# Kernel tuning notes

Measured on AMD Instinct MI355X. Metric: run time of the kernel, lower is better.

Reference implementation:

```python
import jax, jax.numpy as jnp
import numpy as np

HIDDEN = 768

def setup_inputs() -> dict:
    key = jax.random.key(0)
    k1, k2, k3 = jax.random.split(key, 3)
    x = jax.random.normal(k1, (8, 2048, HIDDEN), dtype=jnp.float32)
    # nn.Linear(hidden, 3*hidden): weight [3H, H], bias [3H]; torch init ~ U(-1/sqrt(H), 1/sqrt(H))
    bound = 1.0 / np.sqrt(HIDDEN)
    W = jax.random.uniform(k2, (3 * HIDDEN, HIDDEN), dtype=jnp.float32, minval=-bound, maxval=bound)
    b = jax.random.uniform(k3, (3 * HIDDEN,), dtype=jnp.float32, minval=-bound, maxval=bound)
    return {"x": x, "W": W, "b": b}

def reference(x, W, b):
    # qkv: [B, N, 3H]
    qkv = jnp.einsum('bnd,hd->bnh', x, W) + b
    q, k, v = jnp.split(qkv, 3, axis=-1)  # each [B, N, H]
    # NOTE: original module applies NO 1/sqrt(d) scaling — kept faithful.
    weights = jnp.einsum('bnd,bmd->bnm', q, k)          # [B, N, N]
    weights = jax.nn.softmax(weights, axis=-1)
    out = jnp.einsum('bnm,bmd->bnd', weights, v)        # [B, N, H]
    return out
```

## Files before the change

### kernel.cpp

```cpp
#include <hip/hip_runtime.h>


typedef short    s16x8 __attribute__((ext_vector_type(8)));
typedef _Float16 h16x8 __attribute__((ext_vector_type(8)));
typedef _Float16 h16x4 __attribute__((ext_vector_type(4)));
typedef float    f32x4 __attribute__((ext_vector_type(4)));

__device__ __forceinline__ unsigned short f2bf(float x) {
    unsigned u = __float_as_uint(x);
    u += 0x7fffu + ((u >> 16) & 1u);
    return (unsigned short)(u >> 16);
}
__device__ __forceinline__ float bf2f(unsigned short h) {
    return __uint_as_float(((unsigned)h) << 16);
}
__device__ __forceinline__ unsigned short f2h(float x) {
    _Float16 h = (_Float16)x;
    unsigned short u;
    __builtin_memcpy(&u, &h, 2);
    return u;
}
__device__ __forceinline__ h16x8 as_h(s16x8 v) {
    h16x8 r; __builtin_memcpy(&r, &v, 16); return r;
}

__device__ __forceinline__ void gld16(const void* g, void* l) {
    __builtin_amdgcn_global_load_lds(
        (const __attribute__((address_space(1))) unsigned int*)(unsigned long long)g,
        (__attribute__((address_space(3))) unsigned int*)(unsigned)(unsigned long long)l,
        16, 0, 0);
}

template<bool FP16>
__device__ __forceinline__ f32x4 mma(s16x8 a, s16x8 b, f32x4 c) {
    if constexpr (FP16)
        return __builtin_amdgcn_mfma_f32_16x16x32_f16(as_h(a), as_h(b), c, 0, 0, 0);
    else
        return __builtin_amdgcn_mfma_f32_16x16x32_bf16(a, b, c, 0, 0, 0);
}

template<int MODE, bool FP16, int SWZ>
__global__ __launch_bounds__(512, 2)
void gemm_mfma(const unsigned short* __restrict__ A, const unsigned short* __restrict__ B,
               const float* __restrict__ bias, const float* __restrict__ rvec,
               float* __restrict__ Cf, unsigned short* __restrict__ Ch,
               int K, int lda, int ldb, int ldc,
               long long sA, long long sB, long long sC, long long sR)
{
    __shared__ unsigned short As[4][8192];
    __shared__ unsigned short Bs[4][8192];

    int bx = blockIdx.x, by = blockIdx.y, bz = blockIdx.z;
    if (SWZ == 1) {
        const int l = bx + gridDim.x * (by + gridDim.y * bz);
        bz = l & 7;
        const int t = l >> 3;
        bx = t % gridDim.x;
        by = t / gridDim.x;
    } else if (SWZ == 2) {
        const int l = bx + gridDim.x * by;
        const int c = l & 7;
        const int t = l >> 3;
        const int rows = gridDim.y >> 3;
        bx = t % gridDim.x;
        by = c * rows + t / gridDim.x;
    }

    A += (long long)bz * sA;
    B += (long long)bz * sB;

    const long long m0 = (long long)by * 256;
    const long long n0 = (long long)bx * 256;

    const int tid  = threadIdx.x;
    const int wave = tid >> 6, lane = tid & 63;
    const int wr = wave >> 2, wc = wave & 3;
    const int ml = lane & 15, kq = (lane >> 4) * 8;
    const int srr = wave * 16 + (lane >> 2);
    const int skc = (lane & 3) * 8;

    const int aidx = (wr * 128 + ml) * 32 + kq;
    const int bidx = (wc * 64  + ml) * 32 + kq;

    const unsigned short* Abase = A + (m0 + srr) * (long long)lda + skc;
    const unsigned short* Bbase = B + (n0 + srr) * (long long)ldb + skc;
    const long long a128 = 128LL * lda, b128 = 128LL * ldb;

    auto stage_a = [&](int t, int buf) {
        const unsigned short* p = Abase + t * 32;
        gld16(p,        &As[buf][wave * 512]);
        gld16(p + a128, &As[buf][4096 + wave * 512]);
    };
    auto stage_b = [&](int t, int buf) {
        const unsigned short* p = Bbase + t * 32;
        gld16(p,        &Bs[buf][wave * 512]);
        gld16(p + b128, &Bs[buf][4096 + wave * 512]);
    };

    f32x4 acc[8][4];
#pragma unroll
    for (int i = 0; i < 8; ++i)
#pragma unroll
        for (int j = 0; j < 4; ++j) acc[i][j] = f32x4{0.f, 0.f, 0.f, 0.f};

    const int nt = K >> 5;

    stage_a(0, 0); stage_b(0, 0);
    stage_a(1, 1); stage_b(1, 1);
    stage_a(2, 2); stage_b(2, 2);
    asm volatile("s_waitcnt vmcnt(8)");
    __builtin_amdgcn_s_barrier();

    for (int t = 0; t < nt; ++t) {
        const int cur = t & 3;
        const unsigned short* as = &As[cur][0];
        const unsigned short* bs = &Bs[cur][0];
        const bool pf = (t + 3 < nt);
        const int nb = (t + 3) & 3;

        s16x8 a4[4], b4[4];

#pragma unroll
        for (int i = 0; i < 4; ++i) a4[i] = *(const s16x8*)&as[aidx + i * 512];
#pragma unroll
        for (int j = 0; j < 4; ++j) b4[j] = *(const s16x8*)&bs[bidx + j * 512];
        if (pf) stage_a(t + 3, nb);
        __builtin_amdgcn_s_barrier();
        asm volatile("s_waitcnt lgkmcnt(0)");
        __builtin_amdgcn_sched_barrier(0);
        __builtin_amdgcn_s_setprio(1);
#pragma unroll
        for (int i = 0; i < 4; ++i)
#pragma unroll
            for (int j = 0; j < 4; ++j)
                acc[i][j] = mma<FP16>(a4[i], b4[j], acc[i][j]);
        __builtin_amdgcn_s_setprio(0);
        __builtin_amdgcn_s_barrier();

#pragma unroll
        for (int i = 0; i < 4; ++i) a4[i] = *(const s16x8*)&as[aidx + (i + 4) * 512];
        if (pf) stage_b(t + 3, nb);
        __builtin_amdgcn_s_barrier();
        asm volatile("s_waitcnt lgkmcnt(0)");
        __builtin_amdgcn_sched_barrier(0);
        __builtin_amdgcn_s_setprio(1);
#pragma unroll
        for (int i = 0; i < 4; ++i)
#pragma unroll
            for (int j = 0; j < 4; ++j)
                acc[i + 4][j] = mma<FP16>(a4[i], b4[j], acc[i + 4][j]);
        __builtin_amdgcn_s_setprio(0);
        if (pf)                { asm volatile("s_waitcnt vmcnt(8)"); }
        else if (t + 3 == nt)  { asm volatile("s_waitcnt vmcnt(4)"); }
        else if (t + 2 == nt)  { asm volatile("s_waitcnt vmcnt(0)"); }
        __builtin_amdgcn_s_barrier();
    }

    const int r0 = (lane >> 4) * 4;
    const long long rowbase = m0 + wr * 128 + r0;
    const long long colbase = n0 + wc * 64 + ml;
    if (MODE == 1 || MODE == 2) {
#pragma unroll
        for (int i = 0; i < 8; ++i) {
            const long long rowb = rowbase + i * 16;
#pragma unroll
            for (int j = 0; j < 4; ++j) {
                const long long col = colbase + j * 16;
                const float bj = bias[col];
#pragma unroll
                for (int q = 0; q < 4; ++q) {
                    const float vv = acc[i][j][q] + bj;
                    Ch[(rowb + q) * (long long)ldc + col] = (MODE == 1) ? f2h(vv) : f2bf(vv);
                }
            }
        }
    } else if (MODE == 3) {
        Ch += (long long)bz * sC;
#pragma unroll
        for (int i = 0; i < 8; ++i) {
            const long long rowb = rowbase + i * 16;
#pragma unroll
            for (int j = 0; j < 4; ++j) {
                const long long col = colbase + j * 16;
#pragma unroll
                for (int q = 0; q < 4; ++q)
                    Ch[(rowb + q) * (long long)ldc + col] = f2bf(__expf(acc[i][j][q]));
            }
        }
    } else {
        Cf += (long long)bz * sC;
        rvec += (long long)bz * sR;
#pragma unroll
        for (int i = 0; i < 8; ++i) {
            const long long rowb = rowbase + i * 16;
#pragma unroll
            for (int j = 0; j < 4; ++j) {
                const long long col = colbase + j * 16;
#pragma unroll
                for (int q = 0; q < 4; ++q)
                    Cf[(rowb + q) * (long long)ldc + col] = acc[i][j][q] * rvec[rowb + q];
            }
        }
    }
}

__global__ __launch_bounds__(256)
void cvt_f16(const float* __restrict__ in, unsigned short* __restrict__ out, long long n4)
{
    const long long i = (long long)blockIdx.x * 256 + threadIdx.x;
    if (i >= n4) return;
    const float4 v = ((const float4*)in)[i];
    h16x4 o;
    o.x = (_Float16)v.x; o.y = (_Float16)v.y;
    o.z = (_Float16)v.z; o.w = (_Float16)v.w;
    ((h16x4*)out)[i] = o;
}

__global__ __launch_bounds__(256)
void transpose_v(const unsigned short* __restrict__ v, unsigned short* __restrict__ vt)
{
    __shared__ unsigned short t[32][33];
    const int b = blockIdx.z;
    const int n0 = blockIdx.x * 32, h0 = blockIdx.y * 32;
    const int tx = threadIdx.x, ty = threadIdx.y;
    const unsigned short* src = v + (long long)b * 2048 * 768;
#pragma unroll
    for (int q = 0; q < 4; ++q)
        t[ty + q * 8][tx] = src[(long long)(n0 + ty + q * 8) * 768 + h0 + tx];
    __syncthreads();
    unsigned short* dst = vt + ((long long)b * 768 + h0) * 2048 + n0;
#pragma unroll
    for (int q = 0; q < 4; ++q)
        dst[(long long)(ty + q * 8) * 2048 + tx] = t[tx][ty + q * 8];
}

__global__ __launch_bounds__(256)
void rowsum_recip(const unsigned short* __restrict__ E, float* __restrict__ r)
{
    const long long row = blockIdx.x;
    const int t = threadIdx.x, lane = t & 63, w = t >> 6;
    __shared__ float red[4];
    const uint4 v = ((const uint4*)(E + row * 2048))[t];
    float s = bf2f((unsigned short)(v.x & 0xffff)) + bf2f((unsigned short)(v.x >> 16))
            + bf2f((unsigned short)(v.y & 0xffff)) + bf2f((unsigned short)(v.y >> 16))
            + bf2f((unsigned short)(v.z & 0xffff)) + bf2f((unsigned short)(v.z >> 16))
            + bf2f((unsigned short)(v.w & 0xffff)) + bf2f((unsigned short)(v.w >> 16));
#pragma unroll
    for (int o = 32; o; o >>= 1) s += __shfl_xor(s, o);
    if (lane == 0) red[w] = s;
    __syncthreads();
    if (t == 0) r[row] = 1.f / ((red[0] + red[1]) + (red[2] + red[3]));
}

extern "C" void kernel_launch(void* const* d_in, const int* in_sizes, int n_in,
                              void* d_out, int out_size, void* d_ws, size_t ws_size,
                              hipStream_t stream)
{
    const float* x    = (const float*)d_in[0];
    const float* W    = (const float*)d_in[1];
    const float* bias = (const float*)d_in[2];
    float* out = (float*)d_out;

    char* ws = (char*)d_ws;
    unsigned short* xh = (unsigned short*)ws;
    unsigned short* Wh = (unsigned short*)(ws + 25165824LL);
    unsigned short* qk = (unsigned short*)(ws + 28704768LL);
    unsigned short* v  = (unsigned short*)(ws + 79036416LL);
    unsigned short* vt = (unsigned short*)(ws + 104202240LL);
    unsigned short* E  = (unsigned short*)(ws + 129368064LL);
    float*          r  = (float*)(ws + 196476928LL);

    cvt_f16<<<dim3(12288), dim3(256), 0, stream>>>(x, xh, 3145728LL);
    cvt_f16<<<dim3(1728),  dim3(256), 0, stream>>>(W, Wh, 442368LL);

    gemm_mfma<1, true, 2><<<dim3(6, 64, 1), dim3(512), 0, stream>>>(
        xh, Wh, bias, nullptr, nullptr, qk,
        768, 768, 768, 1536, 0, 0, 0, 0);

    gemm_mfma<2, true, 2><<<dim3(3, 64, 1), dim3(512), 0, stream>>>(
        xh, Wh + 1536LL * 768, bias + 1536, nullptr, nullptr, v,
        768, 768, 768, 768, 0, 0, 0, 0);

    transpose_v<<<dim3(64, 24, 8), dim3(32, 8), 0, stream>>>(v, vt);

    gemm_mfma<3, true, 1><<<dim3(8, 8, 8), dim3(512), 0, stream>>>(
        qk, qk + 768, nullptr, nullptr, nullptr, E,
        768, 1536, 1536, 2048,
        2048LL * 1536, 2048LL * 1536, 2048LL * 2048, 0);

    rowsum_recip<<<dim3(16384), dim3(256), 0, stream>>>(E, r);

    gemm_mfma<4, false, 1><<<dim3(3, 8, 8), dim3(512), 0, stream>>>(
        E, vt, nullptr, r, out, nullptr,
        2048, 2048, 2048, 768,
        2048LL * 2048, 768LL * 2048, 2048LL * 768, 2048);
}
```

Measured before the change: 350.4 us.

## XOR-swizzle LDS tile layout and merge GEMM k-step into single phase

Adds an XOR swizzle of the 8-element k-chunk on both the global-to-LDS staging column and the fragment read index, to reduce LDS bank conflicts on the fragment loads. Also collapses the two-half k-step (four A fragments, barrier, MFMA, reload, barrier, MFMA) into one phase that loads all eight A fragments up front, issues both prefetches, runs all 32 MFMAs and then does a single wait and barrier. This removes barriers per iteration but holds more fragment registers live, which can lower occupancy, and drops the explicit lgkmcnt wait so the compiler has to place it.

```diff
diff --git a/kernel.cpp b/kernel.cpp
--- a/kernel.cpp
+++ b/kernel.cpp
@@ -75,12 +75,13 @@
     const int tid  = threadIdx.x;
     const int wave = tid >> 6, lane = tid & 63;
     const int wr = wave >> 2, wc = wave & 3;
-    const int ml = lane & 15, kq = (lane >> 4) * 8;
+    const int ml = lane & 15;
+    const int ku = (((lane >> 4) ^ ((ml >> 1) & 3)) * 8);
     const int srr = wave * 16 + (lane >> 2);
-    const int skc = (lane & 3) * 8;
-
-    const int aidx = (wr * 128 + ml) * 32 + kq;
-    const int bidx = (wc * 64  + ml) * 32 + kq;
+    const int skc = (((lane & 3) ^ ((lane >> 3) & 3)) * 8);
+
+    const int aidx = (wr * 128 + ml) * 32 + ku;
+    const int bidx = (wc * 64  + ml) * 32 + ku;
 
     const unsigned short* Abase = A + (m0 + srr) * (long long)lda + skc;
     const unsigned short* Bbase = B + (n0 + srr) * (long long)ldb + skc;
@@ -108,8 +109,9 @@
     stage_a(0, 0); stage_b(0, 0);
     stage_a(1, 1); stage_b(1, 1);
     stage_a(2, 2); stage_b(2, 2);
-    asm volatile("s_waitcnt vmcnt(8)");
+    asm volatile("s_waitcnt vmcnt(8)" ::: "memory");
     __builtin_amdgcn_s_barrier();
+    __builtin_amdgcn_sched_barrier(0);
 
     for (int t = 0; t < nt; ++t) {
         const int cur = t & 3;
@@ -118,42 +120,29 @@
         const bool pf = (t + 3 < nt);
         const int nb = (t + 3) & 3;
 
-        s16x8 a4[4], b4[4];
-
-#pragma unroll
-        for (int i = 0; i < 4; ++i) a4[i] = *(const s16x8*)&as[aidx + i * 512];
+        s16x8 a8[8], b4[4];
+#pragma unroll
+        for (int i = 0; i < 4; ++i) a8[i] = *(const s16x8*)&as[aidx + i * 512];
 #pragma unroll
         for (int j = 0; j < 4; ++j) b4[j] = *(const s16x8*)&bs[bidx + j * 512];
-        if (pf) stage_a(t + 3, nb);
+#pragma unroll
+        for (int i = 0; i < 4; ++i) a8[4 + i] = *(const s16x8*)&as[aidx + (i + 4) * 512];
+
+        if (pf) { stage_a(t + 3, nb); stage_b(t + 3, nb); }
+
+        __builtin_amdgcn_s_setprio(1);
+#pragma unroll
+        for (int i = 0; i < 8; ++i)
+#pragma unroll
+            for (int j = 0; j < 4; ++j)
+                acc[i][j] = mma<FP16>(a8[i], b4[j], acc[i][j]);
+        __builtin_amdgcn_s_setprio(0);
+
+        if (pf)                { asm volatile("s_waitcnt vmcnt(8)" ::: "memory"); }
+        else if (t + 3 == nt)  { asm volatile("s_waitcnt vmcnt(4)" ::: "memory"); }
+        else if (t + 2 == nt)  { asm volatile("s_waitcnt vmcnt(0)" ::: "memory"); }
         __builtin_amdgcn_s_barrier();
-        asm volatile("s_waitcnt lgkmcnt(0)");
         __builtin_amdgcn_sched_barrier(0);
-        __builtin_amdgcn_s_setprio(1);
-#pragma unroll
-        for (int i = 0; i < 4; ++i)
-#pragma unroll
-            for (int j = 0; j < 4; ++j)
-                acc[i][j] = mma<FP16>(a4[i], b4[j], acc[i][j]);
-        __builtin_amdgcn_s_setprio(0);
-        __builtin_amdgcn_s_barrier();
-
-#pragma unroll
-        for (int i = 0; i < 4; ++i) a4[i] = *(const s16x8*)&as[aidx + (i + 4) * 512];
-        if (pf) stage_b(t + 3, nb);
-        __builtin_amdgcn_s_barrier();
-        asm volatile("s_waitcnt lgkmcnt(0)");
-        __builtin_amdgcn_sched_barrier(0);
-        __builtin_amdgcn_s_setprio(1);
-#pragma unroll
-        for (int i = 0; i < 4; ++i)
-#pragma unroll
-            for (int j = 0; j < 4; ++j)
-                acc[i + 4][j] = mma<FP16>(a4[i], b4[j], acc[i + 4][j]);
-        __builtin_amdgcn_s_setprio(0);
-        if (pf)                { asm volatile("s_waitcnt vmcnt(8)"); }
-        else if (t + 3 == nt)  { asm volatile("s_waitcnt vmcnt(4)"); }
-        else if (t + 2 == nt)  { asm volatile("s_waitcnt vmcnt(0)"); }
-        __builtin_amdgcn_s_barrier();
     }
 
     const int r0 = (lane >> 4) * 4;
```

Measured after the change: 337.1 us. 3.8% less time.

## Restructure GEMM mainloop to double-buffered 64-wide K tiles with XOR-swizzled LDS

Applied to the files above, without the earlier changes.

Replaces the 4-stage, 32-wide K pipeline with a 2-stage, 64-wide K pipeline. Each 256x256 block tile is split into four 128x128 quadrants that are computed in a ping-pong order, interleaving the loads of the next quadrant with MFMA work. LDS rows are XOR-swizzled to avoid bank conflicts on the 128-byte rows. The per-wave output mapping changes and the epilogues are updated to match. The aim is fewer barriers per K element and fewer LDS bank conflicts, at the cost of a shallower prefetch depth and more complex vmcnt accounting.

```diff
diff --git a/kernel.cpp b/kernel.cpp
--- a/kernel.cpp
+++ b/kernel.cpp
@@ -47,8 +47,8 @@
                int K, int lda, int ldb, int ldc,
                long long sA, long long sB, long long sC, long long sR)
 {
-    __shared__ unsigned short As[4][8192];
-    __shared__ unsigned short Bs[4][8192];
+    __shared__ unsigned short As[2][16384];
+    __shared__ unsigned short Bs[2][16384];
 
     int bx = blockIdx.x, by = blockIdx.y, bz = blockIdx.z;
     if (SWZ == 1) {
@@ -75,132 +75,188 @@
     const int tid  = threadIdx.x;
     const int wave = tid >> 6, lane = tid & 63;
     const int wr = wave >> 2, wc = wave & 3;
-    const int ml = lane & 15, kq = (lane >> 4) * 8;
-    const int srr = wave * 16 + (lane >> 2);
-    const int skc = (lane & 3) * 8;
-
-    const int aidx = (wr * 128 + ml) * 32 + kq;
-    const int bidx = (wc * 64  + ml) * 32 + kq;
-
-    const unsigned short* Abase = A + (m0 + srr) * (long long)lda + skc;
-    const unsigned short* Bbase = B + (n0 + srr) * (long long)ldb + skc;
-    const long long a128 = 128LL * lda, b128 = 128LL * ldb;
-
-    auto stage_a = [&](int t, int buf) {
-        const unsigned short* p = Abase + t * 32;
-        gld16(p,        &As[buf][wave * 512]);
-        gld16(p + a128, &As[buf][4096 + wave * 512]);
+    const int ml = lane & 15, kq4 = lane >> 4;
+    const int ua0 = ((kq4)     ^ (ml & 7)) * 8;
+    const int ua1 = ((4 + kq4) ^ (ml & 7)) * 8;
+    const int srow = lane >> 3;
+    const int skc  = ((lane & 7) ^ srow) * 8;
+
+    const int aoff = (wr * 64 + ml) * 64;
+    const int boff = (wc * 32 + ml) * 64;
+
+    auto stA = [&](int kt, int b, int h) {
+#pragma unroll
+        for (int q = 0; q < 2; ++q)
+            gld16(A + (m0 + h * 128 + q * 64 + wave * 8 + srow) * (long long)lda + kt * 64 + skc,
+                  (char*)&As[b][0] + h * 16384 + q * 8192 + wave * 1024);
     };
-    auto stage_b = [&](int t, int buf) {
-        const unsigned short* p = Bbase + t * 32;
-        gld16(p,        &Bs[buf][wave * 512]);
-        gld16(p + b128, &Bs[buf][4096 + wave * 512]);
+    auto stB = [&](int kt, int b, int h) {
+#pragma unroll
+        for (int q = 0; q < 2; ++q)
+            gld16(B + (n0 + h * 128 + q * 64 + wave * 8 + srow) * (long long)ldb + kt * 64 + skc,
+                  (char*)&Bs[b][0] + h * 16384 + q * 8192 + wave * 1024);
     };
 
-    f32x4 acc[8][4];
-#pragma unroll
-    for (int i = 0; i < 8; ++i)
-#pragma unroll
-        for (int j = 0; j < 4; ++j) acc[i][j] = f32x4{0.f, 0.f, 0.f, 0.f};
-
-    const int nt = K >> 5;
-
-    stage_a(0, 0); stage_b(0, 0);
-    stage_a(1, 1); stage_b(1, 1);
-    stage_a(2, 2); stage_b(2, 2);
-    asm volatile("s_waitcnt vmcnt(8)");
+    f32x4 acc[2][4][4];
+#pragma unroll
+    for (int r = 0; r < 2; ++r)
+#pragma unroll
+        for (int i = 0; i < 4; ++i)
+#pragma unroll
+            for (int j = 0; j < 4; ++j) acc[r][i][j] = f32x4{0.f, 0.f, 0.f, 0.f};
+
+    const int nit = K >> 6;
+
+    stA(0, 0, 0); stB(0, 0, 0); stB(0, 0, 1); stA(0, 0, 1);
+    asm volatile("s_waitcnt vmcnt(4)" ::: "memory");
     __builtin_amdgcn_s_barrier();
-
-    for (int t = 0; t < nt; ++t) {
-        const int cur = t & 3;
+    __builtin_amdgcn_sched_barrier(0);
+
+    s16x8 af[4][2], bf0[2][2], bf1[2][2];
+
+    for (int it = 0; it < nit; ++it) {
+        const int cur = it & 1, nb = cur ^ 1;
         const unsigned short* as = &As[cur][0];
         const unsigned short* bs = &Bs[cur][0];
-        const bool pf = (t + 3 < nt);
-        const int nb = (t + 3) & 3;
-
-        s16x8 a4[4], b4[4];
-
-#pragma unroll
-        for (int i = 0; i < 4; ++i) a4[i] = *(const s16x8*)&as[aidx + i * 512];
-#pragma unroll
-        for (int j = 0; j < 4; ++j) b4[j] = *(const s16x8*)&bs[bidx + j * 512];
-        if (pf) stage_a(t + 3, nb);
-        __builtin_amdgcn_s_barrier();
-        asm volatile("s_waitcnt lgkmcnt(0)");
+        const bool pf = (it + 1 < nit);
+        const int kt1 = it + 1;
+
+#pragma unroll
+        for (int i = 0; i < 4; ++i) {
+            af[i][0] = *(const s16x8*)&as[aoff + i * 1024 + ua0];
+            af[i][1] = *(const s16x8*)&as[aoff + i * 1024 + ua1];
+        }
+#pragma unroll
+        for (int j = 0; j < 2; ++j) {
+            bf0[j][0] = *(const s16x8*)&bs[boff + j * 1024 + ua0];
+            bf0[j][1] = *(const s16x8*)&bs[boff + j * 1024 + ua1];
+        }
+        if (pf) { stA(kt1, nb, 0); stB(kt1, nb, 0); }
+        __builtin_amdgcn_s_barrier();
+        asm volatile("s_waitcnt lgkmcnt(0)" ::: "memory");
         __builtin_amdgcn_sched_barrier(0);
         __builtin_amdgcn_s_setprio(1);
 #pragma unroll
-        for (int i = 0; i < 4; ++i)
-#pragma unroll
-            for (int j = 0; j < 4; ++j)
-                acc[i][j] = mma<FP16>(a4[i], b4[j], acc[i][j]);
+        for (int s = 0; s < 2; ++s)
+#pragma unroll
+            for (int i = 0; i < 4; ++i)
+#pragma unroll
+                for (int j = 0; j < 2; ++j)
+                    acc[0][i][j] = mma<FP16>(af[i][s], bf0[j][s], acc[0][i][j]);
         __builtin_amdgcn_s_setprio(0);
-        __builtin_amdgcn_s_barrier();
-
-#pragma unroll
-        for (int i = 0; i < 4; ++i) a4[i] = *(const s16x8*)&as[aidx + (i + 4) * 512];
-        if (pf) stage_b(t + 3, nb);
-        __builtin_amdgcn_s_barrier();
-        asm volatile("s_waitcnt lgkmcnt(0)");
+        if (pf) { asm volatile("s_waitcnt vmcnt(6)" ::: "memory"); }
+        else    { asm volatile("s_waitcnt vmcnt(2)" ::: "memory"); }
+        __builtin_amdgcn_s_barrier();
+        __builtin_amdgcn_sched_barrier(0);
+
+#pragma unroll
+        for (int j = 0; j < 2; ++j) {
+            bf1[j][0] = *(const s16x8*)&bs[8192 + boff + j * 1024 + ua0];
+            bf1[j][1] = *(const s16x8*)&bs[8192 + boff + j * 1024 + ua1];
+        }
+        if (pf) { stB(kt1, nb, 1); }
+        __builtin_amdgcn_s_barrier();
+        asm volatile("s_waitcnt lgkmcnt(0)" ::: "memory");
         __builtin_amdgcn_sched_barrier(0);
         __builtin_amdgcn_s_setprio(1);
 #pragma unroll
-        for (int i = 0; i < 4; ++i)
-#pragma unroll
-            for (int j = 0; j < 4; ++j)
-                acc[i + 4][j] = mma<FP16>(a4[i], b4[j], acc[i + 4][j]);
+        for (int s = 0; s < 2; ++s)
+#pragma unroll
+            for (int i = 0; i < 4; ++i)
+#pragma unroll
+                for (int j = 0; j < 2; ++j)
+                    acc[0][i][2 + j] = mma<FP16>(af[i][s], bf1[j][s], acc[0][i][2 + j]);
         __builtin_amdgcn_s_setprio(0);
-        if (pf)                { asm volatile("s_waitcnt vmcnt(8)"); }
-        else if (t + 3 == nt)  { asm volatile("s_waitcnt vmcnt(4)"); }
-        else if (t + 2 == nt)  { asm volatile("s_waitcnt vmcnt(0)"); }
-        __builtin_amdgcn_s_barrier();
+        if (pf) { asm volatile("s_waitcnt vmcnt(6)" ::: "memory"); }
+        else    { asm volatile("s_waitcnt vmcnt(0)" ::: "memory"); }
+        __builtin_amdgcn_s_barrier();
+        __builtin_amdgcn_sched_barrier(0);
+
+#pragma unroll
+        for (int i = 0; i < 4; ++i) {
+            af[i][0] = *(const s16x8*)&as[8192 + aoff + i * 1024 + ua0];
+            af[i][1] = *(const s16x8*)&as[8192 + aoff + i * 1024 + ua1];
+        }
+        if (pf) { stA(kt1, nb, 1); }
+        __builtin_amdgcn_s_barrier();
+        asm volatile("s_waitcnt lgkmcnt(0)" ::: "memory");
+        __builtin_amdgcn_sched_barrier(0);
+        __builtin_amdgcn_s_setprio(1);
+#pragma unroll
+        for (int s = 0; s < 2; ++s)
+#pragma unroll
+            for (int i = 0; i < 4; ++i)
+#pragma unroll
+                for (int j = 0; j < 2; ++j)
+                    acc[1][i][2 + j] = mma<FP16>(af[i][s], bf1[j][s], acc[1][i][2 + j]);
+        __builtin_amdgcn_s_setprio(0);
+        __builtin_amdgcn_s_barrier();
+        __builtin_amdgcn_sched_barrier(0);
+
+        __builtin_amdgcn_s_barrier();
+        __builtin_amdgcn_s_setprio(1);
+#pragma unroll
+        for (int s = 0; s < 2; ++s)
+#pragma unroll
+            for (int i = 0; i < 4; ++i)
+#pragma unroll
+                for (int j = 0; j < 2; ++j)
+                    acc[1][i][j] = mma<FP16>(af[i][s], bf0[j][s], acc[1][i][j]);
+        __builtin_amdgcn_s_setprio(0);
+        if (pf) { asm volatile("s_waitcnt vmcnt(4)" ::: "memory"); }
+        __builtin_amdgcn_s_barrier();
+        __builtin_amdgcn_sched_barrier(0);
     }
 
     const int r0 = (lane >> 4) * 4;
-    const long long rowbase = m0 + wr * 128 + r0;
-    const long long colbase = n0 + wc * 64 + ml;
     if (MODE == 1 || MODE == 2) {
 #pragma unroll
-        for (int i = 0; i < 8; ++i) {
-            const long long rowb = rowbase + i * 16;
-#pragma unroll
-            for (int j = 0; j < 4; ++j) {
-                const long long col = colbase + j * 16;
-                const float bj = bias[col];
-#pragma unroll
-                for (int q = 0; q < 4; ++q) {
-                    const float vv = acc[i][j][q] + bj;
-                    Ch[(rowb + q) * (long long)ldc + col] = (MODE == 1) ? f2h(vv) : f2bf(vv);
+        for (int rh = 0; rh < 2; ++rh)
+#pragma unroll
+            for (int i = 0; i < 4; ++i) {
+                const long long rowb = m0 + rh * 128 + wr * 64 + i * 16 + r0;
+#pragma unroll
+                for (int jg = 0; jg < 4; ++jg) {
+                    const long long col = n0 + (jg >> 1) * 128 + wc * 32 + (jg & 1) * 16 + ml;
+                    const float bj = bias[col];
+#pragma unroll
+                    for (int q = 0; q < 4; ++q) {
+                        const float vv = acc[rh][i][jg][q] + bj;
+                        Ch[(rowb + q) * (long long)ldc + col] = (MODE == 1) ? f2h(vv) : f2bf(vv);
+                    }
                 }
             }
-        }
     } else if (MODE == 3) {
         Ch += (long long)bz * sC;
 #pragma unroll
-        for (int i = 0; i < 8; ++i) {
-            const long long rowb = rowbase + i * 16;
-#pragma unroll
-            for (int j = 0; j < 4; ++j) {
-                const long long col = colbase + j * 16;
-#pragma unroll
-                for (int q = 0; q < 4; ++q)
-                    Ch[(rowb + q) * (long long)ldc + col] = f2bf(__expf(acc[i][j][q]));
+        for (int rh = 0; rh < 2; ++rh)
+#pragma unroll
+            for (int i = 0; i < 4; ++i) {
+                const long long rowb = m0 + rh * 128 + wr * 64 + i * 16 + r0;
+#pragma unroll
+                for (int jg = 0; jg < 4; ++jg) {
+                    const long long col = n0 + (jg >> 1) * 128 + wc * 32 + (jg & 1) * 16 + ml;
+#pragma unroll
+                    for (int q = 0; q < 4; ++q)
+                        Ch[(rowb + q) * (long long)ldc + col] = f2bf(__expf(acc[rh][i][jg][q]));
+                }
             }
-        }
     } else {
         Cf += (long long)bz * sC;
         rvec += (long long)bz * sR;
 #pragma unroll
-        for (int i = 0; i < 8; ++i) {
-            const long long rowb = rowbase + i * 16;
-#pragma unroll
-            for (int j = 0; j < 4; ++j) {
-                const long long col = colbase + j * 16;
-#pragma unroll
-                for (int q = 0; q < 4; ++q)
-                    Cf[(rowb + q) * (long long)ldc + col] = acc[i][j][q] * rvec[rowb + q];
+        for (int rh = 0; rh < 2; ++rh)
+#pragma unroll
+            for (int i = 0; i < 4; ++i) {
+                const long long rowb = m0 + rh * 128 + wr * 64 + i * 16 + r0;
+#pragma unroll
+                for (int jg = 0; jg < 4; ++jg) {
+                    const long long col = n0 + (jg >> 1) * 128 + wc * 32 + (jg & 1) * 16 + ml;
+#pragma unroll
+                    for (int q = 0; q < 4; ++q)
+                        Cf[(rowb + q) * (long long)ldc + col] = acc[rh][i][jg][q] * rvec[rowb + q];
+                }
             }
-        }
     }
 }
 
```

After: 326.2 us. -6.9%, faster.
